# Kernel tuning notes

Measured on AMD Instinct MI355X. Metric: run time of the kernel, lower is better.

The kernel has to match this reference:

```python
import jax, jax.numpy as jnp
import numpy as np

FEATURE_DIM = 512


def setup_inputs() -> dict:
    key = jax.random.key(0)
    ks = jax.random.split(key, 12)
    B, Nv, Dv = 32, 1024, 768
    Nl, Dl = 77, 512
    D = FEATURE_DIM
    s = lambda fan_in: 1.0 / np.sqrt(fan_in)
    return {
        "fv": jax.random.normal(ks[0], (B, Nv, Dv), jnp.float32),
        "fl": jax.random.normal(ks[1], (B, Nl, Dl), jnp.float32),
        # linear_vk / linear_vv: Dv -> D (stored as [in, out])
        "W_vk": jax.random.uniform(ks[2], (Dv, D), jnp.float32, -s(Dv), s(Dv)),
        "b_vk": jax.random.uniform(ks[3], (D,), jnp.float32, -s(Dv), s(Dv)),
        "W_vv": jax.random.uniform(ks[4], (Dv, D), jnp.float32, -s(Dv), s(Dv)),
        "b_vv": jax.random.uniform(ks[5], (D,), jnp.float32, -s(Dv), s(Dv)),
        # linear_lk / linear_lv: Dl -> D
        "W_lk": jax.random.uniform(ks[6], (Dl, D), jnp.float32, -s(Dl), s(Dl)),
        "b_lk": jax.random.uniform(ks[7], (D,), jnp.float32, -s(Dl), s(Dl)),
        "W_lv": jax.random.uniform(ks[8], (Dl, D), jnp.float32, -s(Dl), s(Dl)),
        "b_lv": jax.random.uniform(ks[9], (D,), jnp.float32, -s(Dl), s(Dl)),
        # linear_m: nl(77) -> 768
        "W_m": jax.random.uniform(ks[10], (Nl, 768), jnp.float32, -s(Nl), s(Nl)),
        "b_m": jax.random.uniform(ks[11], (768,), jnp.float32, -s(Nl), s(Nl)),
    }


def reference(fv, fl, W_vk, b_vk, W_vv, b_vv, W_lk, b_lk, W_lv, b_lv, W_m, b_m):
    # projections
    fk_v = jnp.einsum("bvd,de->bve", fv, W_vk) + b_vk   # [B, Nv, D]
    fv_v = jnp.einsum("bvd,de->bve", fv, W_vv) + b_vv   # [B, Nv, D]
    fk_l = jnp.einsum("bld,de->ble", fl, W_lk) + b_lk   # [B, Nl, D]
    fv_l = jnp.einsum("bld,de->ble", fl, W_lv) + b_lv   # [B, Nl, D]
    # shared score matrix [B, Nl, Nv]
    a_raw = jnp.einsum("ble,bve->blv", fk_l, fk_v) / jnp.sqrt(
        jnp.asarray(FEATURE_DIM, fk_l.dtype))
    # dual softmax: over Nv for language queries, over Nl for vision queries
    fa_v = jnp.einsum("blv,bve->ble", jax.nn.softmax(a_raw, axis=-1), fv_v)  # [B, Nl, D]
    fa_l = jnp.einsum("bvl,ble->bve",
                      jax.nn.softmax(jnp.swapaxes(a_raw, -1, -2), axis=-1),
                      fv_l)                                                  # [B, Nv, D]
    # fm = fa_v @ fa_l^T -> [B, Nl, Nv]; transpose(1,2) -> [B, Nv, Nl]
    fm = jnp.einsum("bve,ble->bvl", fa_l, fa_v)          # [B, Nv, Nl]
    return jnp.einsum("bvl,lo->bvo", fm, W_m) + b_m      # [B, Nv, 768]
```

## Files before the change

### kernel.cpp

```cpp
#include <hip/hip_runtime.h>


using s16x8  = __attribute__((ext_vector_type(8))) short;
using f32x4v = __attribute__((ext_vector_type(4))) float;

__device__ __forceinline__ unsigned short f2bf(float f) {
  unsigned int u = __float_as_uint(f);
  u += 0x7fffu + ((u >> 16) & 1u);
  return (unsigned short)(u >> 16);
}
__device__ __forceinline__ float bf2f(unsigned short h) {
  return __uint_as_float(((unsigned int)h) << 16);
}
__device__ __forceinline__ void split2(float v, unsigned short &hh, unsigned short &ll) {
  hh = f2bf(v);
  ll = f2bf(v - bf2f(hh));
}
__device__ __forceinline__ void split8(const float* __restrict__ src, s16x8& H, s16x8& L) {
  float4 v0 = *(const float4*)src;
  float4 v1 = *(const float4*)(src + 4);
  unsigned short hh, ll;
  split2(v0.x, hh, ll); H[0] = (short)hh; L[0] = (short)ll;
  split2(v0.y, hh, ll); H[1] = (short)hh; L[1] = (short)ll;
  split2(v0.z, hh, ll); H[2] = (short)hh; L[2] = (short)ll;
  split2(v0.w, hh, ll); H[3] = (short)hh; L[3] = (short)ll;
  split2(v1.x, hh, ll); H[4] = (short)hh; L[4] = (short)ll;
  split2(v1.y, hh, ll); H[5] = (short)hh; L[5] = (short)ll;
  split2(v1.z, hh, ll); H[6] = (short)hh; L[6] = (short)ll;
  split2(v1.w, hh, ll); H[7] = (short)hh; L[7] = (short)ll;
}

__global__ __launch_bounds__(256) void prep_weight(const float* __restrict__ W,
                                                   unsigned short* __restrict__ Wh,
                                                   unsigned short* __restrict__ Wl,
                                                   int K, int N, int Kpad) {
  __shared__ float tile[32][33];
  int nb = blockIdx.x * 32, kb = blockIdx.y * 32;
  int tx = threadIdx.x & 31, ty = threadIdx.x >> 5;
  #pragma unroll
  for (int i = 0; i < 32; i += 8) {
    int k = kb + ty + i, n = nb + tx;
    tile[ty + i][tx] = (k < K && n < N) ? W[(long)k * N + n] : 0.f;
  }
  __syncthreads();
  #pragma unroll
  for (int i = 0; i < 32; i += 8) {
    int n = nb + ty + i, k = kb + tx;
    if (n < N && k < Kpad) {
      unsigned short hh, ll;
      split2(tile[tx][ty + i], hh, ll);
      Wh[(long)n * Kpad + k] = hh;
      Wl[(long)n * Kpad + k] = ll;
    }
  }
}

struct GemmArgs {
  const unsigned short *Ah, *Alo, *Bh, *Blo;
  const float *Af, *Bf;
  int K;
  int Mld, Nld;
  int lda, ldb;
  long long sA, sB;
};

template <bool AF32, bool BF32, class Epi>
__global__ __launch_bounds__(256, 2) void gemm_x3(GemmArgs g, Epi epi) {
  __shared__ __align__(16) unsigned short sm[4 * 128 * 64];
  unsigned short* sAh = sm;
  unsigned short* sAl = sm + 8192;
  unsigned short* sBh = sm + 16384;
  unsigned short* sBl = sm + 24576;

  const int t    = threadIdx.x;
  const int b    = blockIdx.z;
  const int m0   = blockIdx.y * 128;
  const int n0   = blockIdx.x * 128;
  const int lane = t & 63;
  const int w    = t >> 6;
  const int wr   = (w >> 1) * 64;
  const int wc   = (w & 1) * 64;

  const long long aBase = (long long)b * g.sA;
  const long long bBase = (long long)b * g.sB;

  f32x4v acc[4][4];
  #pragma unroll
  for (int i = 0; i < 4; ++i)
    #pragma unroll
    for (int j = 0; j < 4; ++j)
      #pragma unroll
      for (int r = 0; r < 4; ++r) acc[i][j][r] = 0.f;

  const int nkt = g.K >> 6;
  for (int kt = 0; kt < nkt; ++kt) {
    const int k0 = kt << 6;
    if (kt) __syncthreads();
    #pragma unroll
    for (int q = 0; q < 4; ++q) {
      int flat = q * 256 + t;
      int row = flat >> 3, slot = flat & 7;
      int rg = m0 + row; if (rg > g.Mld - 1) rg = g.Mld - 1;
      int doff = row * 64 + ((slot ^ (row & 7)) << 3);
      if constexpr (AF32) {
        const float* src = g.Af + aBase + (long long)rg * g.lda + k0 + (slot << 3);
        s16x8 H, L;
        split8(src, H, L);
        *(s16x8*)&sAh[doff] = H;
        *(s16x8*)&sAl[doff] = L;
      } else {
        long long so = aBase + (long long)rg * g.lda + k0 + (slot << 3);
        *(s16x8*)&sAh[doff] = *(const s16x8*)(g.Ah + so);
        *(s16x8*)&sAl[doff] = *(const s16x8*)(g.Alo + so);
      }
    }
    #pragma unroll
    for (int q = 0; q < 4; ++q) {
      int flat = q * 256 + t;
      int row = flat >> 3, slot = flat & 7;
      int cg = n0 + row; if (cg > g.Nld - 1) cg = g.Nld - 1;
      int doff = row * 64 + ((slot ^ (row & 7)) << 3);
      if constexpr (BF32) {
        const float* src = g.Bf + bBase + (long long)cg * g.ldb + k0 + (slot << 3);
        s16x8 H, L;
        split8(src, H, L);
        *(s16x8*)&sBh[doff] = H;
        *(s16x8*)&sBl[doff] = L;
      } else {
        long long so = bBase + (long long)cg * g.ldb + k0 + (slot << 3);
        *(s16x8*)&sBh[doff] = *(const s16x8*)(g.Bh + so);
        *(s16x8*)&sBl[doff] = *(const s16x8*)(g.Blo + so);
      }
    }
    __syncthreads();
    #pragma unroll
    for (int ks = 0; ks < 2; ++ks) {
      s16x8 ah[4], al[4], bh[4], bl[4];
      #pragma unroll
      for (int i = 0; i < 4; ++i) {
        int row  = wr + i * 16 + (lane & 15);
        int slot = ks * 4 + (lane >> 4);
        int off  = row * 64 + ((slot ^ (row & 7)) << 3);
        ah[i] = *(const s16x8*)&sAh[off];
        al[i] = *(const s16x8*)&sAl[off];
      }
      #pragma unroll
      for (int j = 0; j < 4; ++j) {
        int row  = wc + j * 16 + (lane & 15);
        int slot = ks * 4 + (lane >> 4);
        int off  = row * 64 + ((slot ^ (row & 7)) << 3);
        bh[j] = *(const s16x8*)&sBh[off];
        bl[j] = *(const s16x8*)&sBl[off];
      }
      #pragma unroll
      for (int i = 0; i < 4; ++i)
        #pragma unroll
        for (int j = 0; j < 4; ++j) {
          acc[i][j] = __builtin_amdgcn_mfma_f32_16x16x32_bf16(ah[i], bh[j], acc[i][j], 0, 0, 0);
          acc[i][j] = __builtin_amdgcn_mfma_f32_16x16x32_bf16(ah[i], bl[j], acc[i][j], 0, 0, 0);
          acc[i][j] = __builtin_amdgcn_mfma_f32_16x16x32_bf16(al[i], bh[j], acc[i][j], 0, 0, 0);
        }
    }
  }
  #pragma unroll
  for (int i = 0; i < 4; ++i)
    #pragma unroll
    for (int j = 0; j < 4; ++j) {
      int mm = m0 + wr + i * 16 + ((lane >> 4) << 2);
      int nn = n0 + wc + j * 16 + (lane & 15);
      epi(b, mm, nn, acc[i][j]);
    }
}

struct EpiBF16Pair {
  unsigned short *h, *lo; const float* bias; long long bs; int ld; int Mst;
  __device__ void operator()(int b, int m, int n, f32x4v v) const {
    float bb = bias ? bias[n] : 0.f;
    #pragma unroll
    for (int r = 0; r < 4; ++r) {
      int mm = m + r;
      if (mm < Mst) {
        long long o = (long long)b * bs + (long long)mm * ld + n;
        unsigned short hh, ll;
        split2(v[r] + bb, hh, ll);
        h[o] = hh; lo[o] = ll;
      }
    }
  }
};

struct EpiTransV {
  unsigned short *h, *lo; const float* bias;
  __device__ void operator()(int, int m, int n, f32x4v v) const {
    int b2 = m >> 10, vv = m & 1023;
    float bb = bias[n];
    ushort4 H, L;
    split2(v[0] + bb, H.x, L.x); split2(v[1] + bb, H.y, L.y);
    split2(v[2] + bb, H.z, L.z); split2(v[3] + bb, H.w, L.w);
    long long o = ((long long)b2 * 512 + n) * 1024 + vv;
    *(ushort4*)(h + o)  = H;
    *(ushort4*)(lo + o) = L;
  }
};

struct EpiTransL {
  unsigned short *h, *lo; const float* bias;
  __device__ void operator()(int, int m, int n, f32x4v v) const {
    float bb = bias[n];
    #pragma unroll
    for (int r = 0; r < 4; ++r) {
      int mm = m + r;
      if (mm < 2464) {
        int b2 = mm / 77, l = mm - b2 * 77;
        long long o = ((long long)b2 * 512 + n) * 128 + l;
        unsigned short hh, ll;
        split2(v[r] + bb, hh, ll);
        h[o] = hh; lo[o] = ll;
      }
    }
  }
};

struct EpiScore {
  float* out;
  __device__ void operator()(int b, int m, int n, f32x4v v) const {
    #pragma unroll
    for (int r = 0; r < 4; ++r) {
      int mm = m + r;
      if (mm < 77)
        out[((long long)b * 77 + mm) * 1024 + n] = v[r] * 0.04419417382415922f;
    }
  }
};

struct EpiOut {
  float* out; const float* bias;
  __device__ void operator()(int, int m, int n, f32x4v v) const {
    float bb = bias[n];
    #pragma unroll
    for (int r = 0; r < 4; ++r)
      out[(long long)(m + r) * 768 + n] = v[r] + bb;
  }
};

__global__ __launch_bounds__(256) void softmax_rows(const float* __restrict__ a,
                                                    unsigned short* __restrict__ Ph,
                                                    unsigned short* __restrict__ Plo) {
  long row = blockIdx.x;
  const float* src = a + row * 1024;
  int t = threadIdx.x;
  float4 x = ((const float4*)src)[t];
  float mx = fmaxf(fmaxf(x.x, x.y), fmaxf(x.z, x.w));
  #pragma unroll
  for (int o = 32; o; o >>= 1) mx = fmaxf(mx, __shfl_xor(mx, o));
  __shared__ float red[4], red2[4];
  int w = t >> 6;
  if ((t & 63) == 0) red[w] = mx;
  __syncthreads();
  mx = fmaxf(fmaxf(red[0], red[1]), fmaxf(red[2], red[3]));
  float e0 = __expf(x.x - mx), e1 = __expf(x.y - mx);
  float e2 = __expf(x.z - mx), e3 = __expf(x.w - mx);
  float s = e0 + e1 + e2 + e3;
  #pragma unroll
  for (int o = 32; o; o >>= 1) s += __shfl_xor(s, o);
  if ((t & 63) == 0) red2[w] = s;
  __syncthreads();
  s = red2[0] + red2[1] + red2[2] + red2[3];
  float inv = 1.f / s;
  ushort4 H, L;
  split2(e0 * inv, H.x, L.x); split2(e1 * inv, H.y, L.y);
  split2(e2 * inv, H.z, L.z); split2(e3 * inv, H.w, L.w);
  long o = row * 1024 + (long)t * 4;
  *(ushort4*)(Ph + o)  = H;
  *(ushort4*)(Plo + o) = L;
}

__global__ __launch_bounds__(128) void softmax_cols(const float* __restrict__ a,
                                                    unsigned short* __restrict__ Ph,
                                                    unsigned short* __restrict__ Plo) {
  __shared__ float tile[77 * 129];
  __shared__ float inv[128];
  int t = threadIdx.x;
  int c = blockIdx.x;
  int b = blockIdx.y;
  const float* src = a + (long)b * 77 * 1024 + c * 128;
  for (int r = 0; r < 77; ++r) tile[r * 129 + t] = src[(long)r * 1024 + t];
  __syncthreads();
  float mx = -1e30f;
  for (int r = 0; r < 77; ++r) mx = fmaxf(mx, tile[r * 129 + t]);
  float s = 0.f;
  for (int r = 0; r < 77; ++r) {
    float e = __expf(tile[r * 129 + t] - mx);
    tile[r * 129 + t] = e;
    s += e;
  }
  inv[t] = 1.f / s;
  __syncthreads();
  unsigned short* dh = Ph  + ((long)b * 1024 + c * 128) * 128;
  unsigned short* dl = Plo + ((long)b * 1024 + c * 128) * 128;
  for (int vb = 0; vb < 128; vb += 2) {
    int v = vb + (t >> 6);
    int k = (t & 63) * 2;
    float iv = inv[v];
    float p0 = (k     < 77) ? tile[k * 129 + v] * iv       : 0.f;
    float p1 = (k + 1 < 77) ? tile[(k + 1) * 129 + v] * iv : 0.f;
    ushort2 H, L;
    split2(p0, H.x, L.x); split2(p1, H.y, L.y);
    *(ushort2*)(dh + (long)v * 128 + k) = H;
    *(ushort2*)(dl + (long)v * 128 + k) = L;
  }
}

extern "C" void kernel_launch(void* const* d_in, const int* in_sizes, int n_in,
                              void* d_out, int out_size, void* d_ws, size_t ws_size,
                              hipStream_t stream) {
  const float* fv   = (const float*)d_in[0];
  const float* fl   = (const float*)d_in[1];
  const float* W_vk = (const float*)d_in[2];
  const float* b_vk = (const float*)d_in[3];
  const float* W_vv = (const float*)d_in[4];
  const float* b_vv = (const float*)d_in[5];
  const float* W_lk = (const float*)d_in[6];
  const float* b_lk = (const float*)d_in[7];
  const float* W_lv = (const float*)d_in[8];
  const float* b_lv = (const float*)d_in[9];
  const float* W_m  = (const float*)d_in[10];
  const float* b_m  = (const float*)d_in[11];

  char* base = (char*)d_ws;
  size_t off = 0;
  auto take = [&](size_t bytes) -> char* {
    char* p = base + off;
    off = (off + bytes + 255) & ~(size_t)255;
    return p;
  };

  unsigned short* wvk_h = (unsigned short*)take(786432);
  unsigned short* wvk_l = (unsigned short*)take(786432);
  unsigned short* wvv_h = (unsigned short*)take(786432);
  unsigned short* wvv_l = (unsigned short*)take(786432);
  unsigned short* wlk_h = (unsigned short*)take(524288);
  unsigned short* wlk_l = (unsigned short*)take(524288);
  unsigned short* wlv_h = (unsigned short*)take(524288);
  unsigned short* wlv_l = (unsigned short*)take(524288);
  unsigned short* wm_h  = (unsigned short*)take(196608);
  unsigned short* wm_l  = (unsigned short*)take(196608);
  unsigned short* fkl_h   = (unsigned short*)take(2523136);
  unsigned short* fkl_lo  = (unsigned short*)take(2523136);
  unsigned short* fvlT_h  = (unsigned short*)take(4194304);
  unsigned short* fvlT_lo = (unsigned short*)take(4194304);
  char* regB = take(67108864);
  unsigned short* fkv_h  = (unsigned short*)regB;
  unsigned short* fkv_lo = (unsigned short*)(regB + 33554432);
  unsigned short* p1_h   = (unsigned short*)regB;
  unsigned short* p1_lo  = (unsigned short*)(regB + 5046272);
  unsigned short* p2t_h  = (unsigned short*)(regB + 10092544);
  unsigned short* p2t_lo = (unsigned short*)(regB + 18481152);
  char* regC = take(83886080);
  unsigned short* fvvT_h  = (unsigned short*)regC;
  unsigned short* fvvT_lo = (unsigned short*)(regC + 33554432);
  unsigned short* fal_h   = (unsigned short*)regC;
  unsigned short* fal_lo  = (unsigned short*)(regC + 33554432);
  unsigned short* fm_h    = (unsigned short*)(regC + 67108864);
  unsigned short* fm_lo   = (unsigned short*)(regC + 75497472);
  char* regD = take(10092544);
  float*          araw   = (float*)regD;
  unsigned short* fav_h  = (unsigned short*)regD;
  unsigned short* fav_lo = (unsigned short*)(regD + 4194304);

  if (off > ws_size) return;

  prep_weight<<<dim3(16, 24), 256, 0, stream>>>(W_vk, wvk_h, wvk_l, 768, 512, 768);
  prep_weight<<<dim3(16, 24), 256, 0, stream>>>(W_vv, wvv_h, wvv_l, 768, 512, 768);
  prep_weight<<<dim3(16, 16), 256, 0, stream>>>(W_lk, wlk_h, wlk_l, 512, 512, 512);
  prep_weight<<<dim3(16, 16), 256, 0, stream>>>(W_lv, wlv_h, wlv_l, 512, 512, 512);
  prep_weight<<<dim3(24, 4), 256, 0, stream>>>(W_m, wm_h, wm_l, 77, 768, 128);

  {
    GemmArgs g{}; g.Af = fl; g.Bh = wlk_h; g.Blo = wlk_l;
    g.K = 512; g.Mld = 2464; g.Nld = 512; g.lda = 512; g.ldb = 512; g.sA = 0; g.sB = 0;
    EpiBF16Pair e{fkl_h, fkl_lo, b_lk, 0, 512, 2464};
    gemm_x3<true, false, EpiBF16Pair><<<dim3(4, 20, 1), 256, 0, stream>>>(g, e);
  }
  {
    GemmArgs g{}; g.Af = fl; g.Bh = wlv_h; g.Blo = wlv_l;
    g.K = 512; g.Mld = 2464; g.Nld = 512; g.lda = 512; g.ldb = 512; g.sA = 0; g.sB = 0;
    EpiTransL e{fvlT_h, fvlT_lo, b_lv};
    gemm_x3<true, false, EpiTransL><<<dim3(4, 20, 1), 256, 0, stream>>>(g, e);
  }
  {
    GemmArgs g{}; g.Af = fv; g.Bh = wvk_h; g.Blo = wvk_l;
    g.K = 768; g.Mld = 32768; g.Nld = 512; g.lda = 768; g.ldb = 768; g.sA = 0; g.sB = 0;
    EpiBF16Pair e{fkv_h, fkv_lo, b_vk, 0, 512, 32768};
    gemm_x3<true, false, EpiBF16Pair><<<dim3(4, 256, 1), 256, 0, stream>>>(g, e);
  }
  {
    GemmArgs g{}; g.Af = fv; g.Bh = wvv_h; g.Blo = wvv_l;
    g.K = 768; g.Mld = 32768; g.Nld = 512; g.lda = 768; g.ldb = 768; g.sA = 0; g.sB = 0;
    EpiTransV e{fvvT_h, fvvT_lo, b_vv};
    gemm_x3<true, false, EpiTransV><<<dim3(4, 256, 1), 256, 0, stream>>>(g, e);
  }
  {
    GemmArgs g{}; g.Ah = fkl_h; g.Alo = fkl_lo; g.Bh = fkv_h; g.Blo = fkv_lo;
    g.K = 512; g.Mld = 77; g.Nld = 1024; g.lda = 512; g.ldb = 512;
    g.sA = 77 * 512; g.sB = 1024 * 512;
    EpiScore e{araw};
    gemm_x3<false, false, EpiScore><<<dim3(8, 1, 32), 256, 0, stream>>>(g, e);
  }
  softmax_rows<<<2464, 256, 0, stream>>>(araw, p1_h, p1_lo);
  softmax_cols<<<dim3(8, 32), 128, 0, stream>>>(araw, p2t_h, p2t_lo);
  {
    GemmArgs g{}; g.Ah = p1_h; g.Alo = p1_lo; g.Bh = fvvT_h; g.Blo = fvvT_lo;
    g.K = 1024; g.Mld = 77; g.Nld = 512; g.lda = 1024; g.ldb = 1024;
    g.sA = 77 * 1024; g.sB = 512 * 1024;
    EpiBF16Pair e{fav_h, fav_lo, nullptr, 128 * 512, 512, 128};
    gemm_x3<false, false, EpiBF16Pair><<<dim3(4, 1, 32), 256, 0, stream>>>(g, e);
  }
  {
    GemmArgs g{}; g.Ah = p2t_h; g.Alo = p2t_lo; g.Bh = fvlT_h; g.Blo = fvlT_lo;
    g.K = 128; g.Mld = 1024; g.Nld = 512; g.lda = 128; g.ldb = 128;
    g.sA = 1024 * 128; g.sB = 512 * 128;
    EpiBF16Pair e{fal_h, fal_lo, nullptr, 1024 * 512, 512, 1024};
    gemm_x3<false, false, EpiBF16Pair><<<dim3(4, 8, 32), 256, 0, stream>>>(g, e);
  }
  {
    GemmArgs g{}; g.Ah = fal_h; g.Alo = fal_lo; g.Bh = fav_h; g.Blo = fav_lo;
    g.K = 512; g.Mld = 1024; g.Nld = 128; g.lda = 512; g.ldb = 512;
    g.sA = 1024 * 512; g.sB = 128 * 512;
    EpiBF16Pair e{fm_h, fm_lo, nullptr, 1024 * 128, 128, 1024};
    gemm_x3<false, false, EpiBF16Pair><<<dim3(1, 8, 32), 256, 0, stream>>>(g, e);
  }
  {
    GemmArgs g{}; g.Ah = fm_h; g.Alo = fm_lo; g.Bh = wm_h; g.Blo = wm_l;
    g.K = 128; g.Mld = 32768; g.Nld = 768; g.lda = 128; g.ldb = 128; g.sA = 0; g.sB = 0;
    EpiOut e{(float*)d_out, b_m};
    gemm_x3<false, false, EpiOut><<<dim3(6, 256, 1), 256, 0, stream>>>(g, e);
  }
  (void)in_sizes; (void)n_in; (void)out_size;
}
```

Before: 665.8 us.

## Reassociate tail GEMMs, fuse K/V projections, and double-buffer GEMM loads

The tail chain fa_l·fa_v^T·W_m is reassociated. The small matrix S = fv_l·fa_v^T is computed first, then (S·W_m) is transposed, and a single GEMM applies it to the column-softmax probabilities. This removes the large [B,1024,512] fa_l intermediate and the fm GEMM. The key and value projections now share one GEMM over concatenated weights, with dual epilogues. The GEMM kernel switches to a K=32 tile with register-prefetched, double-buffered shared memory to overlap global loads with MFMA work. The risks are changed rounding from the reassociation and a smaller K step per barrier.

```diff
diff --git a/kernel.cpp b/kernel.cpp
--- a/kernel.cpp
+++ b/kernel.cpp
@@ -16,18 +16,16 @@
   hh = f2bf(v);
   ll = f2bf(v - bf2f(hh));
 }
-__device__ __forceinline__ void split8(const float* __restrict__ src, s16x8& H, s16x8& L) {
-  float4 v0 = *(const float4*)src;
-  float4 v1 = *(const float4*)(src + 4);
+__device__ __forceinline__ void split8v(float4 a, float4 b, s16x8& H, s16x8& L) {
   unsigned short hh, ll;
-  split2(v0.x, hh, ll); H[0] = (short)hh; L[0] = (short)ll;
-  split2(v0.y, hh, ll); H[1] = (short)hh; L[1] = (short)ll;
-  split2(v0.z, hh, ll); H[2] = (short)hh; L[2] = (short)ll;
-  split2(v0.w, hh, ll); H[3] = (short)hh; L[3] = (short)ll;
-  split2(v1.x, hh, ll); H[4] = (short)hh; L[4] = (short)ll;
-  split2(v1.y, hh, ll); H[5] = (short)hh; L[5] = (short)ll;
-  split2(v1.z, hh, ll); H[6] = (short)hh; L[6] = (short)ll;
-  split2(v1.w, hh, ll); H[7] = (short)hh; L[7] = (short)ll;
+  split2(a.x, hh, ll); H[0] = (short)hh; L[0] = (short)ll;
+  split2(a.y, hh, ll); H[1] = (short)hh; L[1] = (short)ll;
+  split2(a.z, hh, ll); H[2] = (short)hh; L[2] = (short)ll;
+  split2(a.w, hh, ll); H[3] = (short)hh; L[3] = (short)ll;
+  split2(b.x, hh, ll); H[4] = (short)hh; L[4] = (short)ll;
+  split2(b.y, hh, ll); H[5] = (short)hh; L[5] = (short)ll;
+  split2(b.z, hh, ll); H[6] = (short)hh; L[6] = (short)ll;
+  split2(b.w, hh, ll); H[7] = (short)hh; L[7] = (short)ll;
 }
 
 __global__ __launch_bounds__(256) void prep_weight(const float* __restrict__ W,
@@ -57,20 +55,16 @@
 
 struct GemmArgs {
   const unsigned short *Ah, *Alo, *Bh, *Blo;
-  const float *Af, *Bf;
+  const float *Af;
   int K;
   int Mld, Nld;
   int lda, ldb;
   long long sA, sB;
 };
 
-template <bool AF32, bool BF32, class Epi>
-__global__ __launch_bounds__(256, 2) void gemm_x3(GemmArgs g, Epi epi) {
-  __shared__ __align__(16) unsigned short sm[4 * 128 * 64];
-  unsigned short* sAh = sm;
-  unsigned short* sAl = sm + 8192;
-  unsigned short* sBh = sm + 16384;
-  unsigned short* sBl = sm + 24576;
+template <bool AF32, class Epi>
+__global__ __launch_bounds__(256, 2) void gemm2(GemmArgs g, Epi epi) {
+  __shared__ __align__(16) unsigned short sm[32768];
 
   const int t    = threadIdx.x;
   const int b    = blockIdx.z;
@@ -84,6 +78,29 @@
   const long long aBase = (long long)b * g.sA;
   const long long bBase = (long long)b * g.sB;
 
+  const int rA0 = t >> 2, rA1 = 64 + (t >> 2), cc = t & 3;
+  const int cOff = cc << 3;
+  int mr0 = m0 + rA0; if (mr0 > g.Mld - 1) mr0 = g.Mld - 1;
+  int mr1 = m0 + rA1; if (mr1 > g.Mld - 1) mr1 = g.Mld - 1;
+  int nr0 = n0 + rA0; if (nr0 > g.Nld - 1) nr0 = g.Nld - 1;
+  int nr1 = n0 + rA1; if (nr1 > g.Nld - 1) nr1 = g.Nld - 1;
+  const long long aR0 = aBase + (long long)mr0 * g.lda;
+  const long long aR1 = aBase + (long long)mr1 * g.lda;
+  const long long bR0 = bBase + (long long)nr0 * g.ldb;
+  const long long bR1 = bBase + (long long)nr1 * g.ldb;
+  const int wA0 = rA0 * 32 + ((cc ^ ((rA0 >> 1) & 3)) << 3);
+  const int wA1 = rA1 * 32 + ((cc ^ ((rA1 >> 1) & 3)) << 3);
+
+  int roffA[4], roffB[4];
+  #pragma unroll
+  for (int i = 0; i < 4; ++i) {
+    int row = wr + i * 16 + (lane & 15);
+    int ch  = lane >> 4;
+    roffA[i] = row * 32 + ((ch ^ ((row >> 1) & 3)) << 3);
+    row = wc + i * 16 + (lane & 15);
+    roffB[i] = row * 32 + ((ch ^ ((row >> 1) & 3)) << 3);
+  }
+
   f32x4v acc[4][4];
   #pragma unroll
   for (int i = 0; i < 4; ++i)
@@ -92,75 +109,72 @@
       #pragma unroll
       for (int r = 0; r < 4; ++r) acc[i][j][r] = 0.f;
 
-  const int nkt = g.K >> 6;
+  float4 pa0, pa1, pa2, pa3;
+  s16x8 pah0, pah1, pal0, pal1;
+  s16x8 pbh0, pbh1, pbl0, pbl1;
+
+  auto issueLoads = [&](int k0) {
+    if constexpr (AF32) {
+      const float* s0 = g.Af + (aR0 + k0 + cOff);
+      const float* s1 = g.Af + (aR1 + k0 + cOff);
+      pa0 = *(const float4*)s0; pa1 = *(const float4*)(s0 + 4);
+      pa2 = *(const float4*)s1; pa3 = *(const float4*)(s1 + 4);
+    } else {
+      pah0 = *(const s16x8*)(g.Ah  + (aR0 + k0 + cOff));
+      pah1 = *(const s16x8*)(g.Ah  + (aR1 + k0 + cOff));
+      pal0 = *(const s16x8*)(g.Alo + (aR0 + k0 + cOff));
+      pal1 = *(const s16x8*)(g.Alo + (aR1 + k0 + cOff));
+    }
+    pbh0 = *(const s16x8*)(g.Bh  + (bR0 + k0 + cOff));
+    pbh1 = *(const s16x8*)(g.Bh  + (bR1 + k0 + cOff));
+    pbl0 = *(const s16x8*)(g.Blo + (bR0 + k0 + cOff));
+    pbl1 = *(const s16x8*)(g.Blo + (bR1 + k0 + cOff));
+  };
+  auto writeStage = [&](int p) {
+    unsigned short* base = sm + p * 16384;
+    if constexpr (AF32) {
+      s16x8 H, L;
+      split8v(pa0, pa1, H, L);
+      *(s16x8*)(base + wA0) = H; *(s16x8*)(base + 4096 + wA0) = L;
+      split8v(pa2, pa3, H, L);
+      *(s16x8*)(base + wA1) = H; *(s16x8*)(base + 4096 + wA1) = L;
+    } else {
+      *(s16x8*)(base + wA0) = pah0; *(s16x8*)(base + wA1) = pah1;
+      *(s16x8*)(base + 4096 + wA0) = pal0; *(s16x8*)(base + 4096 + wA1) = pal1;
+    }
+    *(s16x8*)(base + 8192  + wA0) = pbh0; *(s16x8*)(base + 8192  + wA1) = pbh1;
+    *(s16x8*)(base + 12288 + wA0) = pbl0; *(s16x8*)(base + 12288 + wA1) = pbl1;
+  };
+
+  issueLoads(0);
+  writeStage(0);
+  int p = 0;
+  const int nkt = g.K >> 5;
   for (int kt = 0; kt < nkt; ++kt) {
-    const int k0 = kt << 6;
-    if (kt) __syncthreads();
-    #pragma unroll
-    for (int q = 0; q < 4; ++q) {
-      int flat = q * 256 + t;
-      int row = flat >> 3, slot = flat & 7;
-      int rg = m0 + row; if (rg > g.Mld - 1) rg = g.Mld - 1;
-      int doff = row * 64 + ((slot ^ (row & 7)) << 3);
-      if constexpr (AF32) {
-        const float* src = g.Af + aBase + (long long)rg * g.lda + k0 + (slot << 3);
-        s16x8 H, L;
-        split8(src, H, L);
-        *(s16x8*)&sAh[doff] = H;
-        *(s16x8*)&sAl[doff] = L;
-      } else {
-        long long so = aBase + (long long)rg * g.lda + k0 + (slot << 3);
-        *(s16x8*)&sAh[doff] = *(const s16x8*)(g.Ah + so);
-        *(s16x8*)&sAl[doff] = *(const s16x8*)(g.Alo + so);
-      }
-    }
-    #pragma unroll
-    for (int q = 0; q < 4; ++q) {
-      int flat = q * 256 + t;
-      int row = flat >> 3, slot = flat & 7;
-      int cg = n0 + row; if (cg > g.Nld - 1) cg = g.Nld - 1;
-      int doff = row * 64 + ((slot ^ (row & 7)) << 3);
-      if constexpr (BF32) {
-        const float* src = g.Bf + bBase + (long long)cg * g.ldb + k0 + (slot << 3);
-        s16x8 H, L;
-        split8(src, H, L);
-        *(s16x8*)&sBh[doff] = H;
-        *(s16x8*)&sBl[doff] = L;
-      } else {
-        long long so = bBase + (long long)cg * g.ldb + k0 + (slot << 3);
-        *(s16x8*)&sBh[doff] = *(const s16x8*)(g.Bh + so);
-        *(s16x8*)&sBl[doff] = *(const s16x8*)(g.Blo + so);
-      }
-    }
     __syncthreads();
-    #pragma unroll
-    for (int ks = 0; ks < 2; ++ks) {
-      s16x8 ah[4], al[4], bh[4], bl[4];
-      #pragma unroll
-      for (int i = 0; i < 4; ++i) {
-        int row  = wr + i * 16 + (lane & 15);
-        int slot = ks * 4 + (lane >> 4);
-        int off  = row * 64 + ((slot ^ (row & 7)) << 3);
-        ah[i] = *(const s16x8*)&sAh[off];
-        al[i] = *(const s16x8*)&sAl[off];
-      }
+    if (kt + 1 < nkt) issueLoads((kt + 1) << 5);
+    unsigned short* base = sm + p * 16384;
+    s16x8 ah[4], al[4], bh[4], bl[4];
+    #pragma unroll
+    for (int i = 0; i < 4; ++i) {
+      ah[i] = *(const s16x8*)(base + roffA[i]);
+      al[i] = *(const s16x8*)(base + 4096 + roffA[i]);
+    }
+    #pragma unroll
+    for (int j = 0; j < 4; ++j) {
+      bh[j] = *(const s16x8*)(base + 8192  + roffB[j]);
+      bl[j] = *(const s16x8*)(base + 12288 + roffB[j]);
+    }
+    #pragma unroll
+    for (int i = 0; i < 4; ++i)
       #pragma unroll
       for (int j = 0; j < 4; ++j) {
-        int row  = wc + j * 16 + (lane & 15);
-        int slot = ks * 4 + (lane >> 4);
-        int off  = row * 64 + ((slot ^ (row & 7)) << 3);
-        bh[j] = *(const s16x8*)&sBh[off];
-        bl[j] = *(const s16x8*)&sBl[off];
+        acc[i][j] = __builtin_amdgcn_mfma_f32_16x16x32_bf16(ah[i], bh[j], acc[i][j], 0, 0, 0);
+        acc[i][j] = __builtin_amdgcn_mfma_f32_16x16x32_bf16(ah[i], bl[j], acc[i][j], 0, 0, 0);
+        acc[i][j] = __builtin_amdgcn_mfma_f32_16x16x32_bf16(al[i], bh[j], acc[i][j], 0, 0, 0);
       }
-      #pragma unroll
-      for (int i = 0; i < 4; ++i)
-        #pragma unroll
-        for (int j = 0; j < 4; ++j) {
-          acc[i][j] = __builtin_amdgcn_mfma_f32_16x16x32_bf16(ah[i], bh[j], acc[i][j], 0, 0, 0);
-          acc[i][j] = __builtin_amdgcn_mfma_f32_16x16x32_bf16(ah[i], bl[j], acc[i][j], 0, 0, 0);
-          acc[i][j] = __builtin_amdgcn_mfma_f32_16x16x32_bf16(al[i], bh[j], acc[i][j], 0, 0, 0);
-        }
-    }
+    if (kt + 1 < nkt) writeStage(p ^ 1);
+    p ^= 1;
   }
   #pragma unroll
   for (int i = 0; i < 4; ++i)
@@ -189,34 +203,48 @@
   }
 };
 
-struct EpiTransV {
-  unsigned short *h, *lo; const float* bias;
+struct EpiDualL {
+  unsigned short *kh, *kl, *vh, *vl; const float *bk, *bv;
   __device__ void operator()(int, int m, int n, f32x4v v) const {
-    int b2 = m >> 10, vv = m & 1023;
-    float bb = bias[n];
-    ushort4 H, L;
-    split2(v[0] + bb, H.x, L.x); split2(v[1] + bb, H.y, L.y);
-    split2(v[2] + bb, H.z, L.z); split2(v[3] + bb, H.w, L.w);
-    long long o = ((long long)b2 * 512 + n) * 1024 + vv;
-    *(ushort4*)(h + o)  = H;
-    *(ushort4*)(lo + o) = L;
-  }
-};
-
-struct EpiTransL {
-  unsigned short *h, *lo; const float* bias;
-  __device__ void operator()(int, int m, int n, f32x4v v) const {
-    float bb = bias[n];
+    bool lo512 = n < 512;
+    float bb = lo512 ? bk[n] : bv[n - 512];
+    int nn = lo512 ? n : n - 512;
+    unsigned short* H = lo512 ? kh : vh;
+    unsigned short* L = lo512 ? kl : vl;
     #pragma unroll
     for (int r = 0; r < 4; ++r) {
       int mm = m + r;
       if (mm < 2464) {
-        int b2 = mm / 77, l = mm - b2 * 77;
-        long long o = ((long long)b2 * 512 + n) * 128 + l;
+        long long o = (long long)mm * 512 + nn;
         unsigned short hh, ll;
         split2(v[r] + bb, hh, ll);
-        h[o] = hh; lo[o] = ll;
+        H[o] = hh; L[o] = ll;
       }
+    }
+  }
+};
+
+struct EpiDualV {
+  unsigned short *kh, *kl, *vh, *vl; const float *bk, *bv;
+  __device__ void operator()(int, int m, int n, f32x4v v) const {
+    if (n < 512) {
+      float bb = bk[n];
+      #pragma unroll
+      for (int r = 0; r < 4; ++r) {
+        long long o = (long long)(m + r) * 512 + n;
+        unsigned short hh, ll;
+        split2(v[r] + bb, hh, ll);
+        kh[o] = hh; kl[o] = ll;
+      }
+    } else {
+      int b2 = m >> 10, vv = m & 1023;
+      float bb = bv[n - 512];
+      ushort4 H, L;
+      split2(v[0] + bb, H.x, L.x); split2(v[1] + bb, H.y, L.y);
+      split2(v[2] + bb, H.z, L.z); split2(v[3] + bb, H.w, L.w);
+      long long o = ((long long)b2 * 512 + (n - 512)) * 1024 + vv;
+      *(ushort4*)(vh + o) = H;
+      *(ushort4*)(vl + o) = L;
     }
   }
 };
@@ -233,13 +261,28 @@
   }
 };
 
-struct EpiOut {
+struct EpiTransT {
+  unsigned short *h, *lo;
+  __device__ void operator()(int b, int m, int n, f32x4v v) const {
+    #pragma unroll
+    for (int r = 0; r < 4; ++r) {
+      int mm = m + r;
+      float val = (mm < 77) ? v[r] : 0.f;
+      long long o = (long long)b * 98304 + (long long)n * 128 + mm;
+      unsigned short hh, ll;
+      split2(val, hh, ll);
+      h[o] = hh; lo[o] = ll;
+    }
+  }
+};
+
+struct EpiOutB {
   float* out; const float* bias;
-  __device__ void operator()(int, int m, int n, f32x4v v) const {
+  __device__ void operator()(int b, int m, int n, f32x4v v) const {
     float bb = bias[n];
     #pragma unroll
     for (int r = 0; r < 4; ++r)
-      out[(long long)(m + r) * 768 + n] = v[r] + bb;
+      out[(long long)(b * 1024 + m + r) * 768 + n] = v[r] + bb;
   }
 };
 
@@ -335,106 +378,88 @@
     return p;
   };
 
-  unsigned short* wvk_h = (unsigned short*)take(786432);
-  unsigned short* wvk_l = (unsigned short*)take(786432);
-  unsigned short* wvv_h = (unsigned short*)take(786432);
-  unsigned short* wvv_l = (unsigned short*)take(786432);
-  unsigned short* wlk_h = (unsigned short*)take(524288);
-  unsigned short* wlk_l = (unsigned short*)take(524288);
-  unsigned short* wlv_h = (unsigned short*)take(524288);
-  unsigned short* wlv_l = (unsigned short*)take(524288);
-  unsigned short* wm_h  = (unsigned short*)take(196608);
-  unsigned short* wm_l  = (unsigned short*)take(196608);
-  unsigned short* fkl_h   = (unsigned short*)take(2523136);
-  unsigned short* fkl_lo  = (unsigned short*)take(2523136);
-  unsigned short* fvlT_h  = (unsigned short*)take(4194304);
-  unsigned short* fvlT_lo = (unsigned short*)take(4194304);
-  char* regB = take(67108864);
-  unsigned short* fkv_h  = (unsigned short*)regB;
-  unsigned short* fkv_lo = (unsigned short*)(regB + 33554432);
-  unsigned short* p1_h   = (unsigned short*)regB;
-  unsigned short* p1_lo  = (unsigned short*)(regB + 5046272);
-  unsigned short* p2t_h  = (unsigned short*)(regB + 10092544);
-  unsigned short* p2t_lo = (unsigned short*)(regB + 18481152);
-  char* regC = take(83886080);
-  unsigned short* fvvT_h  = (unsigned short*)regC;
-  unsigned short* fvvT_lo = (unsigned short*)(regC + 33554432);
-  unsigned short* fal_h   = (unsigned short*)regC;
-  unsigned short* fal_lo  = (unsigned short*)(regC + 33554432);
-  unsigned short* fm_h    = (unsigned short*)(regC + 67108864);
-  unsigned short* fm_lo   = (unsigned short*)(regC + 75497472);
-  char* regD = take(10092544);
-  float*          araw   = (float*)regD;
-  unsigned short* fav_h  = (unsigned short*)regD;
-  unsigned short* fav_lo = (unsigned short*)(regD + 4194304);
+  unsigned short* wcatv_h = (unsigned short*)take(1572864);
+  unsigned short* wcatv_l = (unsigned short*)take(1572864);
+  unsigned short* wcatl_h = (unsigned short*)take(1048576);
+  unsigned short* wcatl_l = (unsigned short*)take(1048576);
+  unsigned short* wm_h    = (unsigned short*)take(196608);
+  unsigned short* wm_l    = (unsigned short*)take(196608);
+  unsigned short* fkl_h  = (unsigned short*)take(2523136);
+  unsigned short* fkl_l  = (unsigned short*)take(2523136);
+  unsigned short* fvl_h  = (unsigned short*)take(2523136);
+  unsigned short* fvl_l  = (unsigned short*)take(2523136);
+  unsigned short* fkv_h  = (unsigned short*)take(33554432);
+  unsigned short* fkv_l  = (unsigned short*)take(33554432);
+  unsigned short* fvvT_h = (unsigned short*)take(33554432);
+  unsigned short* fvvT_l = (unsigned short*)take(33554432);
+  float*          araw   = (float*)take(10092544);
+  unsigned short* p1_h   = (unsigned short*)take(5046272);
+  unsigned short* p1_l   = (unsigned short*)take(5046272);
+  unsigned short* p2t_h  = (unsigned short*)take(8388608);
+  unsigned short* p2t_l  = (unsigned short*)take(8388608);
+  unsigned short* fav_h  = (unsigned short*)take(4194304);
+  unsigned short* fav_l  = (unsigned short*)take(4194304);
+  unsigned short* s_h    = (unsigned short*)take(1048576);
+  unsigned short* s_l    = (unsigned short*)take(1048576);
+  unsigned short* tt_h   = (unsigned short*)take(6291456);
+  unsigned short* tt_l   = (unsigned short*)take(6291456);
 
   if (off > ws_size) return;
 
-  prep_weight<<<dim3(16, 24), 256, 0, stream>>>(W_vk, wvk_h, wvk_l, 768, 512, 768);
-  prep_weight<<<dim3(16, 24), 256, 0, stream>>>(W_vv, wvv_h, wvv_l, 768, 512, 768);
-  prep_weight<<<dim3(16, 16), 256, 0, stream>>>(W_lk, wlk_h, wlk_l, 512, 512, 512);
-  prep_weight<<<dim3(16, 16), 256, 0, stream>>>(W_lv, wlv_h, wlv_l, 512, 512, 512);
+  prep_weight<<<dim3(16, 24), 256, 0, stream>>>(W_vk, wcatv_h, wcatv_l, 768, 512, 768);
+  prep_weight<<<dim3(16, 24), 256, 0, stream>>>(W_vv, wcatv_h + 512 * 768, wcatv_l + 512 * 768, 768, 512, 768);
+  prep_weight<<<dim3(16, 16), 256, 0, stream>>>(W_lk, wcatl_h, wcatl_l, 512, 512, 512);
+  prep_weight<<<dim3(16, 16), 256, 0, stream>>>(W_lv, wcatl_h + 512 * 512, wcatl_l + 512 * 512, 512, 512, 512);
   prep_weight<<<dim3(24, 4), 256, 0, stream>>>(W_m, wm_h, wm_l, 77, 768, 128);
 
   {
-    GemmArgs g{}; g.Af = fl; g.Bh = wlk_h; g.Blo = wlk_l;
-    g.K = 512; g.Mld = 2464; g.Nld = 512; g.lda = 512; g.ldb = 512; g.sA = 0; g.sB = 0;
-    EpiBF16Pair e{fkl_h, fkl_lo, b_lk, 0, 512, 2464};
-    gemm_x3<true, false, EpiBF16Pair><<<dim3(4, 20, 1), 256, 0, stream>>>(g, e);
-  }
-  {
-    GemmArgs g{}; g.Af = fl; g.Bh = wlv_h; g.Blo = wlv_l;
-    g.K = 512; g.Mld = 2464; g.Nld = 512; g.lda = 512; g.ldb = 512; g.sA = 0; g.sB = 0;
-    EpiTransL e{fvlT_h, fvlT_lo, b_lv};
-    gemm_x3<true, false, EpiTransL><<<dim3(4, 20, 1), 256, 0, stream>>>(g, e);
-  }
-  {
-    GemmArgs g{}; g.Af = fv; g.Bh = wvk_h; g.Blo = wvk_l;
-    g.K = 768; g.Mld = 32768; g.Nld = 512; g.lda = 768; g.ldb = 768; g.sA = 0; g.sB = 0;
-    EpiBF16Pair e{fkv_h, fkv_lo, b_vk, 0, 512, 32768};
-    gemm_x3<true, false, EpiBF16Pair><<<dim3(4, 256, 1), 256, 0, stream>>>(g, e);
-  }
-  {
-    GemmArgs g{}; g.Af = fv; g.Bh = wvv_h; g.Blo = wvv_l;
-    g.K = 768; g.Mld = 32768; g.Nld = 512; g.lda = 768; g.ldb = 768; g.sA = 0; g.sB = 0;
-    EpiTransV e{fvvT_h, fvvT_lo, b_vv};
-    gemm_x3<true, false, EpiTransV><<<dim3(4, 256, 1), 256, 0, stream>>>(g, e);
-  }
-  {
-    GemmArgs g{}; g.Ah = fkl_h; g.Alo = fkl_lo; g.Bh = fkv_h; g.Blo = fkv_lo;
+    GemmArgs g{}; g.Af = fl; g.Bh = wcatl_h; g.Blo = wcatl_l;
+    g.K = 512; g.Mld = 2464; g.Nld = 1024; g.lda = 512; g.ldb = 512; g.sA = 0; g.sB = 0;
+    EpiDualL e{fkl_h, fkl_l, fvl_h, fvl_l, b_lk, b_lv};
+    gemm2<true, EpiDualL><<<dim3(8, 20, 1), 256, 0, stream>>>(g, e);
+  }
+  {
+    GemmArgs g{}; g.Af = fv; g.Bh = wcatv_h; g.Blo = wcatv_l;
+    g.K = 768; g.Mld = 32768; g.Nld = 1024; g.lda = 768; g.ldb = 768; g.sA = 0; g.sB = 0;
+    EpiDualV e{fkv_h, fkv_l, fvvT_h, fvvT_l, b_vk, b_vv};
+    gemm2<true, EpiDualV><<<dim3(8, 256, 1), 256, 0, stream>>>(g, e);
+  }
+  {
+    GemmArgs g{}; g.Ah = fkl_h; g.Alo = fkl_l; g.Bh = fkv_h; g.Blo = fkv_l;
     g.K = 512; g.Mld = 77; g.Nld = 1024; g.lda = 512; g.ldb = 512;
     g.sA = 77 * 512; g.sB = 1024 * 512;
     EpiScore e{araw};
-    gemm_x3<false, false, EpiScore><<<dim3(8, 1, 32), 256, 0, stream>>>(g, e);
-  }
-  softmax_rows<<<2464, 256, 0, stream>>>(araw, p1_h, p1_lo);
-  softmax_cols<<<dim3(8, 32), 128, 0, stream>>>(araw, p2t_h, p2t_lo);
-  {
-    GemmArgs g{}; g.Ah = p1_h; g.Alo = p1_lo; g.Bh = fvvT_h; g.Blo = fvvT_lo;
+    gemm2<false, EpiScore><<<dim3(8, 1, 32), 256, 0, stream>>>(g, e);
+  }
+  softmax_rows<<<2464, 256, 0, stream>>>(araw, p1_h, p1_l);
+  softmax_cols<<<dim3(8, 32), 128, 0, stream>>>(araw, p2t_h, p2t_l);
+  {
+    GemmArgs g{}; g.Ah = p1_h; g.Alo = p1_l; g.Bh = fvvT_h; g.Blo = fvvT_l;
     g.K = 1024; g.Mld = 77; g.Nld = 512; g.lda = 1024; g.ldb = 1024;
     g.sA = 77 * 1024; g.sB = 512 * 1024;
-    EpiBF16Pair e{fav_h, fav_lo, nullptr, 128 * 512, 512, 128};
-    gemm_x3<false, false, EpiBF16Pair><<<dim3(4, 1, 32), 256, 0, stream>>>(g, e);
-  }
-  {
-    GemmArgs g{}; g.Ah = p2t_h; g.Alo = p2t_lo; g.Bh = fvlT_h; g.Blo = fvlT_lo;
-    g.K = 128; g.Mld = 1024; g.Nld = 512; g.lda = 128; g.ldb = 128;
-    g.sA = 1024 * 128; g.sB = 512 * 128;
-    EpiBF16Pair e{fal_h, fal_lo, nullptr, 1024 * 512, 512, 1024};
-    gemm_x3<false, false, EpiBF16Pair><<<dim3(4, 8, 32), 256, 0, stream>>>(g, e);
-  }
-  {
-    GemmArgs g{}; g.Ah = fal_h; g.Alo = fal_lo; g.Bh = fav_h; g.Blo = fav_lo;
-    g.K = 512; g.Mld = 1024; g.Nld = 128; g.lda = 512; g.ldb = 512;
-    g.sA = 1024 * 512; g.sB = 128 * 512;
-    EpiBF16Pair e{fm_h, fm_lo, nullptr, 1024 * 128, 128, 1024};
-    gemm_x3<false, false, EpiBF16Pair><<<dim3(1, 8, 32), 256, 0, stream>>>(g, e);
-  }
-  {
-    GemmArgs g{}; g.Ah = fm_h; g.Alo = fm_lo; g.Bh = wm_h; g.Blo = wm_l;
-    g.K = 128; g.Mld = 32768; g.Nld = 768; g.lda = 128; g.ldb = 128; g.sA = 0; g.sB = 0;
-    EpiOut e{(float*)d_out, b_m};
-    gemm_x3<false, false, EpiOut><<<dim3(6, 256, 1), 256, 0, stream>>>(g, e);
+    EpiBF16Pair e{fav_h, fav_l, nullptr, 128 * 512, 512, 128};
+    gemm2<false, EpiBF16Pair><<<dim3(4, 1, 32), 256, 0, stream>>>(g, e);
+  }
+  {
+    GemmArgs g{}; g.Ah = fvl_h; g.Alo = fvl_l; g.Bh = fav_h; g.Blo = fav_l;
+    g.K = 512; g.Mld = 77; g.Nld = 128; g.lda = 512; g.ldb = 512;
+    g.sA = 77 * 512; g.sB = 128 * 512;
+    EpiBF16Pair e{s_h, s_l, nullptr, 128 * 128, 128, 128};
+    gemm2<false, EpiBF16Pair><<<dim3(1, 1, 32), 256, 0, stream>>>(g, e);
+  }
+  {
+    GemmArgs g{}; g.Ah = s_h; g.Alo = s_l; g.Bh = wm_h; g.Blo = wm_l;
+    g.K = 128; g.Mld = 128; g.Nld = 768; g.lda = 128; g.ldb = 128;
+    g.sA = 128 * 128; g.sB = 0;
+    EpiTransT e{tt_h, tt_l};
+    gemm2<false, EpiTransT><<<dim3(6, 1, 32), 256, 0, stream>>>(g, e);
+  }
+  {
+    GemmArgs g{}; g.Ah = p2t_h; g.Alo = p2t_l; g.Bh = tt_h; g.Blo = tt_l;
+    g.K = 128; g.Mld = 1024; g.Nld = 768; g.lda = 128; g.ldb = 128;
+    g.sA = 1024 * 128; g.sB = 768 * 128;
+    EpiOutB e{(float*)d_out, b_m};
+    gemm2<false, EpiOutB><<<dim3(6, 8, 32), 256, 0, stream>>>(g, e);
   }
   (void)in_sizes; (void)n_in; (void)out_size;
 }
```

After: 591.0 us. -11.2%, faster.
